# Kernel optimization log

Measured on AMD Instinct MI355X. Metric: run time of the kernel, lower is better.

Reference implementation:

```python
import jax, jax.numpy as jnp
import numpy as np

B, N, C, H = 16, 577, 768, 12  # batch, tokens (HW+1), channels, heads
DH = C // H
FF = 4 * C
EPS = 1e-5  # torch LayerNorm default


def layer_norm(x, g, b):
    mu = jnp.mean(x, axis=-1, keepdims=True)
    var = jnp.mean(jnp.square(x - mu), axis=-1, keepdims=True)
    return (x - mu) * jax.lax.rsqrt(var + EPS) * g + b


def setup_inputs() -> dict:
    key = jax.random.key(0)
    ks = jax.random.split(key, 12)
    s = 0.02
    return {
        "x": jax.random.normal(ks[0], (B, N, C), jnp.float32),
        "_EB": 0,
        "ln1_g": jnp.ones((C,), jnp.float32),
        "ln1_b": jnp.zeros((C,), jnp.float32),
        "wq": jax.random.normal(ks[1], (C, C), jnp.float32) * s,
        "bq": jnp.zeros((C,), jnp.float32),
        "wk": jax.random.normal(ks[2], (C, C), jnp.float32) * s,
        "bk": jnp.zeros((C,), jnp.float32),
        "wv": jax.random.normal(ks[3], (C, C), jnp.float32) * s,
        "bv": jnp.zeros((C,), jnp.float32),
        "wo": jax.random.normal(ks[4], (C, C), jnp.float32) * s,
        "bo": jnp.zeros((C,), jnp.float32),
        "ln2_g": jnp.ones((C,), jnp.float32),
        "ln2_b": jnp.zeros((C,), jnp.float32),
        "w1": jax.random.normal(ks[5], (C, FF), jnp.float32) * s,
        "b1": jax.random.normal(ks[6], (FF,), jnp.float32) * 1e-6,
        "w2": jax.random.normal(ks[7], (FF, C), jnp.float32) * s,
        "b2": jax.random.normal(ks[8], (C,), jnp.float32) * 1e-6,
    }


def reference(x, _EB, ln1_g, ln1_b, wq, bq, wk, bk, wv, bv, wo, bo, ln2_g, ln2_b, w1, b1, w2, b2):
    # pre-norm 1 (_EB is falsy -> skipped, as in the original `if _EB:`)
    h = layer_norm(x, ln1_g, ln1_b)
    # MHSA: naive QK^T -> softmax -> V (the original materializes the full matrix)
    q = (h @ wq + bq).reshape(B, N, H, DH).transpose(0, 2, 1, 3)  # (B,H,N,DH)
    k = (h @ wk + bk).reshape(B, N, H, DH).transpose(0, 2, 1, 3)
    v = (h @ wv + bv).reshape(B, N, H, DH).transpose(0, 2, 1, 3)
    sim = jnp.einsum("bhqd,bhkd->bhqk", q, k) / jnp.sqrt(jnp.float32(DH))
    attn = jax.nn.softmax(sim, axis=-1)  # (B,H,N,N)
    o = jnp.einsum("bhqk,bhkd->bhqd", attn, v)
    o = o.transpose(0, 2, 1, 3).reshape(B, N, C) @ wo + bo
    x1 = x + o
    # pre-norm 2 + GELU MLP (torch nn.GELU default = exact erf gelu)
    h2 = layer_norm(x1, ln2_g, ln2_b)
    m = jax.nn.gelu(h2 @ w1 + b1, approximate=False) @ w2 + b2
    return x1 + m
```

## Files before the change

### kernel.cpp

```cpp
#include <hip/hip_runtime.h>
#include <hip/hip_bf16.h>

#define BATCH 16
#define SEQ   577
#define CDIM  768
#define HEADS 12
#define DHEAD 64
#define FFDIM 3072
#define MROWS (BATCH*SEQ)

typedef __bf16 bf16x8 __attribute__((ext_vector_type(8)));
typedef float  f32x4  __attribute__((ext_vector_type(4)));
typedef unsigned short u16x8 __attribute__((ext_vector_type(8)));

__device__ __forceinline__ unsigned short f2bf(float f) {
    unsigned u = __builtin_bit_cast(unsigned, f);
    unsigned r = (u + 0x7FFFu + ((u >> 16) & 1u)) >> 16;
    return (unsigned short)r;
}
__device__ __forceinline__ float bf2f(unsigned short s) {
    return __builtin_bit_cast(float, (unsigned)s << 16);
}
__device__ __forceinline__ float gelu_f(float v) {
    return 0.5f * v * (1.f + erff(v * 0.7071067811865475f));
}
__device__ __forceinline__ void gll16(const void* g, void* l) {
    __builtin_amdgcn_global_load_lds(
        (const __attribute__((address_space(1))) unsigned int*)g,
        (__attribute__((address_space(3))) unsigned int*)l, 16, 0, 0);
}
#define MFMA16(a, b, c) __builtin_amdgcn_mfma_f32_16x16x32_bf16((a), (b), (c), 0, 0, 0)

#define S0 (2304*768)
#define S1 (768*768)
#define S2 (768*3072)
#define S3 (3072*768)
#define STOT (S0+S1+S2+S3)

__global__ __launch_bounds__(256) void convert_w(
    const float* __restrict__ wq, const float* __restrict__ wk, const float* __restrict__ wv,
    const float* __restrict__ wo, const float* __restrict__ w1, const float* __restrict__ w2,
    const float* __restrict__ bq, const float* __restrict__ bk, const float* __restrict__ bv,
    unsigned short* __restrict__ wqkvT, unsigned short* __restrict__ woT,
    unsigned short* __restrict__ w1T, unsigned short* __restrict__ w2T,
    float* __restrict__ bqkv)
{
    for (size_t id = (size_t)blockIdx.x * 256 + threadIdx.x; id < STOT + 2304; id += (size_t)gridDim.x * 256) {
        if (id < S0) {
            int n = (int)(id / 768), k = (int)(id % 768);
            const float* w = (n < 768) ? wq : (n < 1536) ? wk : wv;
            int c = (n < 768) ? n : (n < 1536) ? n - 768 : n - 1536;
            wqkvT[id] = f2bf(w[(size_t)k * 768 + c]);
        } else if (id < S0 + S1) {
            size_t i2 = id - S0; int n = (int)(i2 / 768), k = (int)(i2 % 768);
            woT[i2] = f2bf(wo[(size_t)k * 768 + n]);
        } else if (id < S0 + S1 + S2) {
            size_t i3 = id - S0 - S1; int n = (int)(i3 / 768), k = (int)(i3 % 768);
            w1T[i3] = f2bf(w1[(size_t)k * 3072 + n]);
        } else if (id < STOT) {
            size_t i4 = id - S0 - S1 - S2; int n = (int)(i4 / 3072), k = (int)(i4 % 3072);
            w2T[i4] = f2bf(w2[(size_t)k * 768 + n]);
        } else {
            int c = (int)(id - STOT);
            float v = (c < 768) ? bq[c] : (c < 1536) ? bk[c - 768] : bv[c - 1536];
            bqkv[c] = v;
        }
    }
}

__global__ __launch_bounds__(256) void ln_bf16(
    const float* __restrict__ x, const float* __restrict__ g, const float* __restrict__ b,
    unsigned short* __restrict__ out)
{
    int row = blockIdx.x;
    int t = threadIdx.x;
    const float* xr = x + (size_t)row * CDIM;
    float v0 = xr[t], v1 = xr[t + 256], v2 = xr[t + 512];
    float s = v0 + v1 + v2;
    float q = v0 * v0 + v1 * v1 + v2 * v2;
    __shared__ float red[8];
    for (int o = 32; o > 0; o >>= 1) { s += __shfl_down(s, o); q += __shfl_down(q, o); }
    int wid = t >> 6;
    if ((t & 63) == 0) { red[wid] = s; red[4 + wid] = q; }
    __syncthreads();
    if (t == 0) {
        float S = red[0] + red[1] + red[2] + red[3];
        float Q = red[4] + red[5] + red[6] + red[7];
        float mu = S * (1.f / CDIM);
        float var = Q * (1.f / CDIM) - mu * mu;
        red[0] = mu; red[1] = rsqrtf(var + 1e-5f);
    }
    __syncthreads();
    float mu = red[0], rs = red[1];
    unsigned short* orow = out + (size_t)row * CDIM;
    orow[t]       = f2bf((v0 - mu) * rs * g[t]       + b[t]);
    orow[t + 256] = f2bf((v1 - mu) * rs * g[t + 256] + b[t + 256]);
    orow[t + 512] = f2bf((v2 - mu) * rs * g[t + 512] + b[t + 512]);
}

template<int EPI>
__global__ __launch_bounds__(256, 2) void gemm128(
    const unsigned short* __restrict__ A, const unsigned short* __restrict__ Bt,
    const float* __restrict__ bias, void* __restrict__ Cout,
    const float* __restrict__ resid, int M, int Nn, int K)
{
    __shared__ __align__(16) unsigned short As[2][128][32];
    __shared__ __align__(16) unsigned short Bs[2][128][32];

    int t = threadIdx.x;
    int gx = gridDim.x;
    int nwg = gx * gridDim.y;
    int bid = blockIdx.y * gx + blockIdx.x;
    int qc = nwg >> 3, rc = nwg & 7;
    int xcd = bid & 7, loc = bid >> 3;
    int swz = (xcd < rc ? xcd * (qc + 1) : rc * (qc + 1) + (xcd - rc) * qc) + loc;
    int nbase = (swz % gx) * 128;
    int mbase = (swz / gx) * 128;

    int lane = t & 63, w = t >> 6;
    int wm = w >> 1, wn = w & 1;
    int lr = lane & 15, lk = lane >> 4;
    int k0 = lk * 8;

    int srow = lane >> 2;
    int scol = (lane & 3) * 8;

    int arow0 = min(mbase + (w * 2    ) * 16 + srow, M - 1);
    int arow1 = min(mbase + (w * 2 + 1) * 16 + srow, M - 1);
    int brow0 = nbase + (w * 2    ) * 16 + srow;
    int brow1 = nbase + (w * 2 + 1) * 16 + srow;
    const unsigned short* ap0 = A  + (size_t)arow0 * K + scol;
    const unsigned short* ap1 = A  + (size_t)arow1 * K + scol;
    const unsigned short* bp0 = Bt + (size_t)brow0 * K + scol;
    const unsigned short* bp1 = Bt + (size_t)brow1 * K + scol;
    char* lA0[2] = { (char*)&As[0][0][0] + (w * 2) * 1024, (char*)&As[1][0][0] + (w * 2) * 1024 };
    char* lB0[2] = { (char*)&Bs[0][0][0] + (w * 2) * 1024, (char*)&Bs[1][0][0] + (w * 2) * 1024 };

    f32x4 acc[4][4] = {};

    gll16(ap0, lA0[0]);
    gll16(ap1, lA0[0] + 1024);
    gll16(bp0, lB0[0]);
    gll16(bp1, lB0[0] + 1024);

    for (int kt = 0; kt < K; kt += 32) {
        int buf = (kt >> 5) & 1;
        __syncthreads();
        if (kt + 32 < K) {
            gll16(ap0 + kt + 32, lA0[buf ^ 1]);
            gll16(ap1 + kt + 32, lA0[buf ^ 1] + 1024);
            gll16(bp0 + kt + 32, lB0[buf ^ 1]);
            gll16(bp1 + kt + 32, lB0[buf ^ 1] + 1024);
        }
        bf16x8 af[4], bfv[4];
#pragma unroll
        for (int mi = 0; mi < 4; mi++) af[mi]  = *(const bf16x8*)&As[buf][wm * 64 + mi * 16 + lr][k0];
#pragma unroll
        for (int ni = 0; ni < 4; ni++) bfv[ni] = *(const bf16x8*)&Bs[buf][wn * 64 + ni * 16 + lr][k0];
#pragma unroll
        for (int mi = 0; mi < 4; mi++)
#pragma unroll
            for (int ni = 0; ni < 4; ni++)
                acc[mi][ni] = MFMA16(af[mi], bfv[ni], acc[mi][ni]);
    }

#pragma unroll
    for (int mi = 0; mi < 4; mi++) {
#pragma unroll
        for (int ni = 0; ni < 4; ni++) {
            int col = nbase + wn * 64 + ni * 16 + lr;
            float bcol = bias[col];
#pragma unroll
            for (int i = 0; i < 4; i++) {
                int row = mbase + wm * 64 + mi * 16 + lk * 4 + i;
                if (row >= M) continue;
                float v = acc[mi][ni][i] + bcol;
                if (EPI == 0) {
                    ((unsigned short*)Cout)[(size_t)row * Nn + col] = f2bf(v);
                } else if (EPI == 1) {
                    ((float*)Cout)[(size_t)row * Nn + col] = resid[(size_t)row * Nn + col] + v;
                } else {
                    ((unsigned short*)Cout)[(size_t)row * Nn + col] = f2bf(gelu_f(v));
                }
            }
        }
    }
}

__global__ __launch_bounds__(256) void attn_kernel(
    const unsigned short* __restrict__ qkv, unsigned short* __restrict__ attno)
{
    int bh = blockIdx.y;
    int b = bh / HEADS, h = bh % HEADS;
    int qt = blockIdx.x;
    int t = threadIdx.x;
    int lane = t & 63, w = t >> 6;
    int lr = lane & 15, lk = lane >> 4, k0 = lk * 8;

    const size_t baseRow = (size_t)b * SEQ;
    const unsigned short* Qp = qkv + baseRow * 2304 + h * 64;
    const unsigned short* Kp = Qp + 768;
    const unsigned short* Vp = Qp + 1536;

    __shared__ __align__(16) unsigned short sSP[32][648];
    __shared__ __align__(16) unsigned short sVt[64 * 64];
    __shared__ float sRedM[4][32];
    __shared__ float sRedS[4][32];

    bf16x8 afr[2][2];
#pragma unroll
    for (int mi = 0; mi < 2; mi++) {
        int qr = qt * 32 + mi * 16 + lr; if (qr > SEQ - 1) qr = SEQ - 1;
#pragma unroll
        for (int ks = 0; ks < 2; ks++)
            afr[mi][ks] = *(const bf16x8*)(Qp + (size_t)qr * 2304 + ks * 32 + k0);
    }
    int jp = t >> 3;
    int dg = (t & 7) * 8;
    u16x8 vA, vB;
    vA = *(const u16x8*)(Vp + (size_t)min(jp * 2,     SEQ - 1) * 2304 + dg);
    vB = *(const u16x8*)(Vp + (size_t)min(jp * 2 + 1, SEQ - 1) * 2304 + dg);

    f32x4 acc[10][2];
    float mx[2][4];
#pragma unroll
    for (int mi = 0; mi < 2; mi++)
#pragma unroll
        for (int i = 0; i < 4; i++) mx[mi][i] = -1e30f;

#pragma unroll
    for (int it = 0; it < 10; it++) {
        int jt = w + it * 4;
        int col = jt * 16 + lr;
        int j = min(col, SEQ - 1);
        f32x4 a0 = {}, a1 = {};
#pragma unroll
        for (int ks = 0; ks < 2; ks++) {
            bf16x8 bfr = *(const bf16x8*)(Kp + (size_t)j * 2304 + ks * 32 + k0);
            a0 = MFMA16(afr[0][ks], bfr, a0);
            a1 = MFMA16(afr[1][ks], bfr, a1);
        }
        acc[it][0] = a0; acc[it][1] = a1;
        if (col < SEQ) {
#pragma unroll
            for (int i = 0; i < 4; i++) {
                mx[0][i] = fmaxf(mx[0][i], a0[i]);
                mx[1][i] = fmaxf(mx[1][i], a1[i]);
            }
        }
    }
#pragma unroll
    for (int mi = 0; mi < 2; mi++) {
#pragma unroll
        for (int i = 0; i < 4; i++) {
            float v = mx[mi][i];
            v = fmaxf(v, __shfl_xor(v, 1));
            v = fmaxf(v, __shfl_xor(v, 2));
            v = fmaxf(v, __shfl_xor(v, 4));
            v = fmaxf(v, __shfl_xor(v, 8));
            mx[mi][i] = v;
        }
    }
    if (lr == 0)
#pragma unroll
        for (int mi = 0; mi < 2; mi++)
#pragma unroll
            for (int i = 0; i < 4; i++)
                sRedM[w][mi * 16 + lk * 4 + i] = mx[mi][i];
    __syncthreads();

    float rm[2][4], sm[2][4];
#pragma unroll
    for (int mi = 0; mi < 2; mi++)
#pragma unroll
        for (int i = 0; i < 4; i++) {
            int ri = mi * 16 + lk * 4 + i;
            rm[mi][i] = fmaxf(fmaxf(sRedM[0][ri], sRedM[1][ri]),
                              fmaxf(sRedM[2][ri], sRedM[3][ri]));
            sm[mi][i] = 0.f;
        }
#pragma unroll
    for (int it = 0; it < 10; it++) {
        int jt = w + it * 4;
        int col = jt * 16 + lr;
        bool valid = col < SEQ;
#pragma unroll
        for (int mi = 0; mi < 2; mi++) {
#pragma unroll
            for (int i = 0; i < 4; i++) {
                float p = valid ? __expf(0.125f * (acc[it][mi][i] - rm[mi][i])) : 0.f;
                sm[mi][i] += p;
                sSP[mi * 16 + lk * 4 + i][col] = f2bf(p);
            }
        }
    }
#pragma unroll
    for (int mi = 0; mi < 2; mi++) {
#pragma unroll
        for (int i = 0; i < 4; i++) {
            float v = sm[mi][i];
            v += __shfl_xor(v, 1);
            v += __shfl_xor(v, 2);
            v += __shfl_xor(v, 4);
            v += __shfl_xor(v, 8);
            sm[mi][i] = v;
        }
    }
    if (lr == 0)
#pragma unroll
        for (int mi = 0; mi < 2; mi++)
#pragma unroll
            for (int i = 0; i < 4; i++)
                sRedS[w][mi * 16 + lk * 4 + i] = sm[mi][i];
    __syncthreads();

    f32x4 oacc[2] = {};
    int d = w * 16 + lr;
    int fx = ((d & 7) ^ (d >> 3)) << 4;
    for (int jc = 0; jc < 10; jc++) {
        __syncthreads();
#pragma unroll
        for (int e = 0; e < 8; e++) {
            unsigned val = (unsigned)vA[e] | ((unsigned)vB[e] << 16);
            int r = dg + e;
            int off = (r * 128 + jp * 4) ^ ((((r & 7) ^ (r >> 3)) & 7) << 4);
            *(unsigned*)((char*)sVt + off) = val;
        }
        if (jc < 9) {
            int j0 = (jc + 1) * 64 + jp * 2;
            vA = *(const u16x8*)(Vp + (size_t)min(j0,     SEQ - 1) * 2304 + dg);
            vB = *(const u16x8*)(Vp + (size_t)min(j0 + 1, SEQ - 1) * 2304 + dg);
        }
        __syncthreads();
#pragma unroll
        for (int ks = 0; ks < 2; ks++) {
            bf16x8 vb = *(const bf16x8*)((char*)sVt + ((d * 128 + ks * 64 + lk * 16) ^ fx));
#pragma unroll
            for (int mi = 0; mi < 2; mi++) {
                bf16x8 pa = *(const bf16x8*)&sSP[mi * 16 + lr][jc * 64 + ks * 32 + k0];
                oacc[mi] = MFMA16(pa, vb, oacc[mi]);
            }
        }
    }

#pragma unroll
    for (int mi = 0; mi < 2; mi++) {
#pragma unroll
        for (int i = 0; i < 4; i++) {
            int ri = mi * 16 + lk * 4 + i;
            int qr = qt * 32 + ri;
            if (qr < SEQ) {
                float rs = sRedS[0][ri] + sRedS[1][ri] + sRedS[2][ri] + sRedS[3][ri];
                float ov = oacc[mi][i] / rs;
                attno[(baseRow + qr) * CDIM + h * 64 + w * 16 + lr] = f2bf(ov);
            }
        }
    }
}

extern "C" void kernel_launch(void* const* d_in, const int* in_sizes, int n_in,
                              void* d_out, int out_size, void* d_ws, size_t ws_size,
                              hipStream_t stream) {
    const float* x     = (const float*)d_in[0];
    const float* ln1_g = (const float*)d_in[2];
    const float* ln1_b = (const float*)d_in[3];
    const float* wq    = (const float*)d_in[4];
    const float* bq    = (const float*)d_in[5];
    const float* wk    = (const float*)d_in[6];
    const float* bk    = (const float*)d_in[7];
    const float* wv    = (const float*)d_in[8];
    const float* bv    = (const float*)d_in[9];
    const float* wo    = (const float*)d_in[10];
    const float* bo    = (const float*)d_in[11];
    const float* ln2_g = (const float*)d_in[12];
    const float* ln2_b = (const float*)d_in[13];
    const float* w1    = (const float*)d_in[14];
    const float* b1    = (const float*)d_in[15];
    const float* w2    = (const float*)d_in[16];
    const float* b2    = (const float*)d_in[17];
    float* out = (float*)d_out;

    char* ws = (char*)d_ws;
    unsigned short* wqkvT = (unsigned short*)(ws + 0);
    unsigned short* woT   = (unsigned short*)(ws + 3538944);
    unsigned short* w1T   = (unsigned short*)(ws + 4718592);
    unsigned short* w2T   = (unsigned short*)(ws + 9437184);
    float*          bqkv  = (float*)         (ws + 14155776);
    unsigned short* qkv   = (unsigned short*)(ws + 14164992);
    unsigned short* hbuf  = (unsigned short*)(ws + 56706048);
    unsigned short* attno = (unsigned short*)(ws + 70886400);
    unsigned short* mid   = (unsigned short*)(ws + 14164992);
    unsigned short* h2    = attno;

    convert_w<<<4096, 256, 0, stream>>>(wq, wk, wv, wo, w1, w2, bq, bk, bv,
                                        wqkvT, woT, w1T, w2T, bqkv);
    ln_bf16<<<MROWS, 256, 0, stream>>>(x, ln1_g, ln1_b, hbuf);
    gemm128<0><<<dim3(2304 / 128, (MROWS + 127) / 128), 256, 0, stream>>>(
        hbuf, wqkvT, bqkv, qkv, nullptr, MROWS, 2304, 768);
    attn_kernel<<<dim3(19, BATCH * HEADS), 256, 0, stream>>>(qkv, attno);
    gemm128<1><<<dim3(768 / 128, (MROWS + 127) / 128), 256, 0, stream>>>(
        attno, woT, bo, out, x, MROWS, 768, 768);
    ln_bf16<<<MROWS, 256, 0, stream>>>(out, ln2_g, ln2_b, h2);
    gemm128<2><<<dim3(3072 / 128, (MROWS + 127) / 128), 256, 0, stream>>>(
        h2, w1T, b1, mid, nullptr, MROWS, 3072, 768);
    gemm128<1><<<dim3(768 / 128, (MROWS + 127) / 128), 256, 0, stream>>>(
        mid, w2T, b2, out, out, MROWS, 768, 3072);
}
```

Baseline: 390.6 us.

## Triple-buffer GEMM LDS tiles with explicit vmcnt waits and prefetch depth 3

Moves the bf16 GEMM main loop from double buffering with one syncthreads per K-step to a three-stage LDS ring. Global-to-LDS loads are issued three tiles ahead, and explicit s_waitcnt vmcnt counts plus raw s_barrier calls replace the full sync. The goal is to hide global load latency behind MFMA work. In exchange, LDS use grows by half, there are two barriers per iteration, and the hand-tuned waitcnt counts assume exactly four outstanding loads per stage.

```diff
diff --git a/kernel.cpp b/kernel.cpp
--- a/kernel.cpp
+++ b/kernel.cpp
@@ -104,8 +104,8 @@
     const float* __restrict__ bias, void* __restrict__ Cout,
     const float* __restrict__ resid, int M, int Nn, int K)
 {
-    __shared__ __align__(16) unsigned short As[2][128][32];
-    __shared__ __align__(16) unsigned short Bs[2][128][32];
+    __shared__ __align__(16) unsigned short As[3][128][32];
+    __shared__ __align__(16) unsigned short Bs[3][128][32];
 
     int t = threadIdx.x;
     int gx = gridDim.x;
@@ -133,36 +133,52 @@
     const unsigned short* ap1 = A  + (size_t)arow1 * K + scol;
     const unsigned short* bp0 = Bt + (size_t)brow0 * K + scol;
     const unsigned short* bp1 = Bt + (size_t)brow1 * K + scol;
-    char* lA0[2] = { (char*)&As[0][0][0] + (w * 2) * 1024, (char*)&As[1][0][0] + (w * 2) * 1024 };
-    char* lB0[2] = { (char*)&Bs[0][0][0] + (w * 2) * 1024, (char*)&Bs[1][0][0] + (w * 2) * 1024 };
+
+    const int nt = K >> 5;
+
+#define STAGE(tk, buf)                                                        \
+    {                                                                         \
+        gll16(ap0 + (tk) * 32, (char*)&As[buf][0][0] + (w * 2    ) * 1024);   \
+        gll16(ap1 + (tk) * 32, (char*)&As[buf][0][0] + (w * 2 + 1) * 1024);   \
+        gll16(bp0 + (tk) * 32, (char*)&Bs[buf][0][0] + (w * 2    ) * 1024);   \
+        gll16(bp1 + (tk) * 32, (char*)&Bs[buf][0][0] + (w * 2 + 1) * 1024);   \
+    }
 
     f32x4 acc[4][4] = {};
 
-    gll16(ap0, lA0[0]);
-    gll16(ap1, lA0[0] + 1024);
-    gll16(bp0, lB0[0]);
-    gll16(bp1, lB0[0] + 1024);
-
-    for (int kt = 0; kt < K; kt += 32) {
-        int buf = (kt >> 5) & 1;
-        __syncthreads();
-        if (kt + 32 < K) {
-            gll16(ap0 + kt + 32, lA0[buf ^ 1]);
-            gll16(ap1 + kt + 32, lA0[buf ^ 1] + 1024);
-            gll16(bp0 + kt + 32, lB0[buf ^ 1]);
-            gll16(bp1 + kt + 32, lB0[buf ^ 1] + 1024);
-        }
+    STAGE(0, 0);
+    if (nt > 1) STAGE(1, 1);
+    if (nt > 2) STAGE(2, 2);
+
+    int c = 0;
+    for (int tk = 0; tk < nt; ++tk) {
+        if (tk + 2 < nt)      { asm volatile("s_waitcnt vmcnt(8)" ::: "memory"); }
+        else if (tk + 1 < nt) { asm volatile("s_waitcnt vmcnt(4)" ::: "memory"); }
+        else                  { asm volatile("s_waitcnt vmcnt(0)" ::: "memory"); }
+        __builtin_amdgcn_sched_barrier(0);
+        __builtin_amdgcn_s_barrier();
+
         bf16x8 af[4], bfv[4];
 #pragma unroll
-        for (int mi = 0; mi < 4; mi++) af[mi]  = *(const bf16x8*)&As[buf][wm * 64 + mi * 16 + lr][k0];
-#pragma unroll
-        for (int ni = 0; ni < 4; ni++) bfv[ni] = *(const bf16x8*)&Bs[buf][wn * 64 + ni * 16 + lr][k0];
+        for (int mi = 0; mi < 4; mi++) af[mi]  = *(const bf16x8*)&As[c][wm * 64 + mi * 16 + lr][k0];
+#pragma unroll
+        for (int ni = 0; ni < 4; ni++) bfv[ni] = *(const bf16x8*)&Bs[c][wn * 64 + ni * 16 + lr][k0];
+        __builtin_amdgcn_sched_barrier(0);
+        asm volatile("s_waitcnt lgkmcnt(0)" ::: "memory");
+        __builtin_amdgcn_sched_barrier(0);
+        __builtin_amdgcn_s_barrier();
+
+        if (tk + 3 < nt) STAGE(tk + 3, c);
+
 #pragma unroll
         for (int mi = 0; mi < 4; mi++)
 #pragma unroll
             for (int ni = 0; ni < 4; ni++)
                 acc[mi][ni] = MFMA16(af[mi], bfv[ni], acc[mi][ni]);
-    }
+
+        c = (c == 2) ? 0 : c + 1;
+    }
+#undef STAGE
 
 #pragma unroll
     for (int mi = 0; mi < 4; mi++) {
```

Result: slower. 403.7 us (+3.3%).
